# Kernel tuning notes

Measured on AMD Instinct MI355X. Metric: run time of the kernel, lower is better.

Reference implementation:

```python
import jax, jax.numpy as jnp
import numpy as np

GAMMA = 1.0          # softmin temperature (module default gamma=1.0)
BIG = 1e30           # finite stand-in for +inf (avoids NaN grads through masked cells)
# step_sizes = [[1,0],[0,1],[1,1]], global_step_weights = [1,1,1], normalization='N'

B, N, M, D = 64, 512, 512, 128


def setup_inputs() -> dict:
    key = jax.random.key(0)
    k1, k2 = jax.random.split(key)
    X = jax.random.normal(k1, (B, N, D), dtype=jnp.float32)
    Y = jax.random.normal(k2, (B, M, D), dtype=jnp.float32)
    return {"X": X, "Y": Y}


def _mse_cost(X, Y):
    # C[b,n,m] = mean_d (X[b,n,d] - Y[b,m,d])^2, expanded to avoid a BxNxMxD intermediate
    d = X.shape[-1]
    x2 = jnp.sum(X * X, axis=-1)                      # (B, N)
    y2 = jnp.sum(Y * Y, axis=-1)                      # (B, M)
    xy = jnp.einsum('bnd,bmd->bnm', X, Y)             # (B, N, M)
    return (x2[:, :, None] + y2[:, None, :] - 2.0 * xy) / d


def _soft_dtw(C):
    # Soft-DTW DP via anti-diagonal wavefront scan.
    # R[n,m] = softmin_gamma(R[n-1,m]+c, R[n,m-1]+c, R[n-1,m-1]+c), R[0,0]=C[0,0]
    # (all global step weights are 1.0). Returns R[N-1, M-1] per batch element.
    b, n, m = C.shape
    i_idx = jnp.arange(n)
    ds = jnp.arange(n + m - 1)
    cols = ds[:, None] - i_idx[None, :]               # (n+m-1, n): col index on each diagonal
    valid = (cols >= 0) & (cols < m)
    colsc = jnp.clip(cols, 0, m - 1)
    Cs = C[:, i_idx[None, :], colsc]                  # (b, n+m-1, n) skewed cost
    Cs = jnp.where(valid[None], Cs, 0.0)
    Cs = jnp.transpose(Cs, (1, 0, 2))                 # (n+m-1, b, n)

    pad = jnp.full((b, 1), BIG, C.dtype)

    def shift(r):  # access index i-1 along the diagonal
        return jnp.concatenate([pad, r[:, :-1]], axis=1)

    def step(carry, inp):
        prev, prev2 = carry                           # diagonals d-1, d-2: (b, n)
        c, val, d = inp
        # candidates: steps (1,0), (0,1), (1,1)
        a = jnp.stack([shift(prev) + c, prev + c, shift(prev2) + c], axis=0)  # (3, b, n)
        mn = jax.lax.stop_gradient(jnp.min(a, axis=0))
        r = mn - GAMMA * jnp.log(jnp.sum(jnp.exp((mn - a) / GAMMA), axis=0))
        # start boundary condition (0,0) with W_start=1
        r = jnp.where((d == 0) & (i_idx[None, :] == 0), c, r)
        r = jnp.where(val[None, :], r, BIG)
        return (r, prev), None

    init = (jnp.full((b, n), BIG, C.dtype), jnp.full((b, n), BIG, C.dtype))
    (last, _), _ = jax.lax.scan(step, init, (Cs, valid, ds))
    # end boundary (N-1, M-1) with additive W_end=0
    return last[:, n - 1]


def reference(X, Y):
    C = _mse_cost(X, Y)
    cost = _soft_dtw(C)                               # (B,)
    # normalization='N': mean over batch of cost / N
    return jnp.mean(cost / X.shape[1])
```

## Files before the change

kernel.cpp:

```cpp
#include <hip/hip_runtime.h>
#include <math.h>

#define BATCH 64
#define NN 512
#define MM 512
#define DD 128
#define BIGF 1e30f
#define KLOG2E 1.442695040888963f
#define LN2F   0.693147180559945f
#define BIGK   (BIGF * KLOG2E)

#define NA 768
#define NP 256

typedef __attribute__((ext_vector_type(2))) float f32x2;
typedef __attribute__((ext_vector_type(4))) float f32x4;
typedef __attribute__((ext_vector_type(8))) short s16x8;

__device__ __forceinline__ unsigned short f2bf(float f) {
    unsigned u = __float_as_uint(f);
    u += 0x7FFFu + ((u >> 16) & 1u);
    return (unsigned short)(u >> 16);
}

#define LSI(A, IP) ((A) * 32 + ((IP) ^ ((A) & 31)))

__global__ __launch_bounds__(256) void cost_diag_mfma(const float* __restrict__ X,
                                                      const float* __restrict__ Y,
                                                      f32x2* __restrict__ Cd) {
    __shared__ alignas(16) short smem[2 * 64 * 128];
    __shared__ float x2s[64];
    __shared__ float y2s[64];
    short* Xbf = smem;
    short* Ybf = smem + 64 * 128;
    f32x2* Ls  = (f32x2*)smem;

    int b  = blockIdx.z;
    int ti = blockIdx.y * 64;
    int tj = blockIdx.x * 64;
    int t  = threadIdx.x;
    int l  = t & 63;
    int w  = t >> 6;

    const float* Xb = X + ((size_t)b * NN + ti) * DD;
    const float* Yb = Y + ((size_t)b * MM + tj) * DD;

    int rw  = t >> 4;
    int k8l = t & 15;
    float xs_acc[4], ys_acc[4];
    #pragma unroll
    for (int it = 0; it < 4; ++it) {
        int r = rw + it * 16;
        const float* sx = Xb + (size_t)r * DD + k8l * 8;
        const float* sy = Yb + (size_t)r * DD + k8l * 8;
        float4 x0 = *(const float4*)sx;
        float4 x1 = *(const float4*)(sx + 4);
        float4 y0 = *(const float4*)sy;
        float4 y1 = *(const float4*)(sy + 4);
        xs_acc[it] = x0.x*x0.x + x0.y*x0.y + x0.z*x0.z + x0.w*x0.w
                   + x1.x*x1.x + x1.y*x1.y + x1.z*x1.z + x1.w*x1.w;
        ys_acc[it] = y0.x*y0.x + y0.y*y0.y + y0.z*y0.z + y0.w*y0.w
                   + y1.x*y1.x + y1.y*y1.y + y1.z*y1.z + y1.w*y1.w;
        s16x8 xv, yv;
        xv[0] = (short)f2bf(x0.x); xv[1] = (short)f2bf(x0.y);
        xv[2] = (short)f2bf(x0.z); xv[3] = (short)f2bf(x0.w);
        xv[4] = (short)f2bf(x1.x); xv[5] = (short)f2bf(x1.y);
        xv[6] = (short)f2bf(x1.z); xv[7] = (short)f2bf(x1.w);
        yv[0] = (short)f2bf(y0.x); yv[1] = (short)f2bf(y0.y);
        yv[2] = (short)f2bf(y0.z); yv[3] = (short)f2bf(y0.w);
        yv[4] = (short)f2bf(y1.x); yv[5] = (short)f2bf(y1.y);
        yv[6] = (short)f2bf(y1.z); yv[7] = (short)f2bf(y1.w);
        int sw = (r * 16 + (k8l ^ (r & 7))) * 8;
        *(s16x8*)&Xbf[sw] = xv;
        *(s16x8*)&Ybf[sw] = yv;
    }
    #pragma unroll
    for (int it = 0; it < 4; ++it) {
        float xs = xs_acc[it], ys = ys_acc[it];
        #pragma unroll
        for (int m = 8; m >= 1; m >>= 1) {
            xs += __shfl_xor(xs, m, 16);
            ys += __shfl_xor(ys, m, 16);
        }
        if (k8l == 0) { x2s[rw + it * 16] = xs; y2s[rw + it * 16] = ys; }
    }
    __syncthreads();

    f32x4 acc0 = {0.f,0.f,0.f,0.f}, acc1 = acc0, acc2 = acc0, acc3 = acc0;
    int ar = 16 * w + (l & 15);
    int kb = l >> 4;
    int c0 = l & 15;
    #pragma unroll
    for (int kk = 0; kk < 4; ++kk) {
        int k8 = kk * 4 + kb;
        s16x8 af = *(const s16x8*)&Xbf[(ar * 16 + (k8 ^ (ar & 7))) * 8];
        s16x8 b0 = *(const s16x8*)&Ybf[((c0     ) * 16 + (k8 ^ ((c0     ) & 7))) * 8];
        s16x8 b1 = *(const s16x8*)&Ybf[((c0 + 16) * 16 + (k8 ^ ((c0 + 16) & 7))) * 8];
        s16x8 b2 = *(const s16x8*)&Ybf[((c0 + 32) * 16 + (k8 ^ ((c0 + 32) & 7))) * 8];
        s16x8 b3 = *(const s16x8*)&Ybf[((c0 + 48) * 16 + (k8 ^ ((c0 + 48) & 7))) * 8];
        acc0 = __builtin_amdgcn_mfma_f32_16x16x32_bf16(af, b0, acc0, 0, 0, 0);
        acc1 = __builtin_amdgcn_mfma_f32_16x16x32_bf16(af, b1, acc1, 0, 0, 0);
        acc2 = __builtin_amdgcn_mfma_f32_16x16x32_bf16(af, b2, acc2, 0, 0, 0);
        acc3 = __builtin_amdgcn_mfma_f32_16x16x32_bf16(af, b3, acc3, 0, 0, 0);
    }

    const float inv = KLOG2E / (float)DD;
    int i0l = 16 * w + (l >> 4) * 4;
    float4 xx = *(const float4*)&x2s[i0l];
    float yy0 = y2s[c0];
    float yy1 = y2s[16 + c0];
    float yy2 = y2s[32 + c0];
    float yy3 = y2s[48 + c0];

    __syncthreads();

    int ipl0 = i0l >> 1;
    #define WRT(ACC, YY, C) do {                                               \
        int jl = 16 * (C) + c0;                                                \
        float v0 = (xx.x + (YY) - 2.0f * (ACC)[0]) * inv;                      \
        float v1 = (xx.y + (YY) - 2.0f * (ACC)[1]) * inv;                      \
        float v2 = (xx.z + (YY) - 2.0f * (ACC)[2]) * inv;                      \
        float v3 = (xx.w + (YY) - 2.0f * (ACC)[3]) * inv;                      \
        Ls[LSI(ipl0 + jl, ipl0)]         = f32x2{v0, v1};                      \
        Ls[LSI(ipl0 + 1 + jl, ipl0 + 1)] = f32x2{v2, v3};                      \
    } while (0)
    WRT(acc0, yy0, 0); WRT(acc1, yy1, 1); WRT(acc2, yy2, 2); WRT(acc3, yy3, 3);
    #undef WRT
    __syncthreads();

    f32x2* Cdb = Cd + (size_t)b * (NA * NP);
    int base_a = (ti >> 1) + tj;
    int ipbase = (ti >> 1);
    #pragma unroll
    for (int k = 0; k < 12; ++k) {
        int f  = t + k * 256;
        int al = f >> 5;
        int il = f & 31;
        int d  = al - il;
        if ((unsigned)d < 64u)
            Cdb[(size_t)(base_a + al) * NP + ipbase + il] = Ls[LSI(al, il)];
    }
}

#define RING 8
#define KCH 16
#define ESK 15
#define NITER 51

__global__ __launch_bounds__(256, 1) void sdtw_diag_kernel(const f32x2* __restrict__ Cd,
                                                           float* __restrict__ part) {
    int b = blockIdx.x;
    int p = threadIdx.x;
    int l = p & 63;
    int w = p >> 6;
    int wm1 = (w == 0) ? 0 : (w - 1);
    int wsk = ESK * w;
    int off = p + wsk;
    const char* CbL = (const char*)Cd + (size_t)b * (NA * NP * 8) + p * 8;

    __shared__ alignas(16) f32x2 buf[2][4][KCH];

    if (p < 128) ((f32x2*)buf)[p] = f32x2{BIGK, 1.0f};
    __syncthreads();

    float ps0 = BIGK, pq0 = 1.0f;
    float ps1 = BIGK, pq1 = 1.0f;
    float nbc_s = BIGK, nbc_q = 1.0f;
    float nbp_s = BIGK, nbp_q = 1.0f;
    f32x2 carry = {BIGK, 1.0f};

    f32x2 b0, b1, b2, b3, b4, b5, b6, b7, b8, b9, b10, b11, b12, b13, b14, b15;
    b0=b1=b2=b3=b4=b5=b6=b7=b8=b9=b10=b11=b12=b13=b14=b15 = f32x2{BIGK, 1.0f};

    f32x2 r0, r1, r2, r3, r4, r5, r6, r7;

#define LOADPD(REG, AV) do {                                                   \
    int a_ = (AV);                                                             \
    a_ = a_ < 0 ? 0 : (a_ > NA - 1 ? NA - 1 : a_);                             \
    const char* pa_ = CbL + (unsigned)a_ * (NP * 8u);                          \
    asm volatile("global_load_dwordx2 %0, %1, off"                             \
                 : "=&v"(REG) : "v"(pa_) : "memory");                          \
} while (0)

    LOADPD(r0, 0 - wsk); LOADPD(r1, 1 - wsk); LOADPD(r2, 2 - wsk);
    LOADPD(r3, 3 - wsk); LOADPD(r4, 4 - wsk); LOADPD(r5, 5 - wsk);
    LOADPD(r6, 6 - wsk); LOADPD(r7, 7 - wsk);

#define STEPD(REG, SIG, BS, UBX, UBY, DBX, DBY) do {                           \
    int s_ = sbase + (SIG);                                                    \
    int j_ = s_ - off;                                                         \
    f32x2 cc;                                                                  \
    asm volatile("s_waitcnt vmcnt(7)" : "=v"(cc) : "0"(REG));                  \
    float su, qu, sd2, qd;                                                     \
    if (l == 0) {                                                              \
        if (w == 0) { su = BIGK; qu = 1.0f;                                    \
                      sd2 = (s_ == 0) ? 0.0f : BIGK; qd = 1.0f; }              \
        else        { su = (UBX); qu = (UBY); sd2 = (DBX); qd = (DBY); }       \
    } else { su = nbc_s; qu = nbc_q; sd2 = nbp_s; qd = nbp_q; }                \
    if ((unsigned)j_ < 512u) {                                                 \
        float lAs = ps0, lAq = pq0;                                            \
        float m1;                                                              \
        asm("v_min3_f32 %0, %1, %2, %3" : "=v"(m1) : "v"(su), "v"(lAs), "v"(sd2)); \
        float eu, el, ed;                                                      \
        asm("v_exp_f32 %0, %1" : "=v"(eu) : "v"(m1 - su));                     \
        asm("v_exp_f32 %0, %1" : "=v"(el) : "v"(m1 - lAs));                    \
        asm("v_exp_f32 %0, %1" : "=v"(ed) : "v"(m1 - sd2));                    \
        float qA = __builtin_fmaf(qu, eu, __builtin_fmaf(lAq, el, qd * ed));   \
        float sA = cc.x + m1;                                                  \
        float m2;                                                              \
        asm("v_min3_f32 %0, %1, %2, %3" : "=v"(m2) : "v"(sA), "v"(ps1), "v"(lAs)); \
        float fu, fl, fd;                                                      \
        asm("v_exp_f32 %0, %1" : "=v"(fu) : "v"(m2 - sA));                     \
        asm("v_exp_f32 %0, %1" : "=v"(fl) : "v"(m2 - ps1));                    \
        asm("v_exp_f32 %0, %1" : "=v"(fd) : "v"(m2 - lAs));                    \
        float qB = __builtin_fmaf(qA, fu, __builtin_fmaf(pq1, fl, lAq * fd));  \
        float sB = cc.y + m2;                                                  \
        ps0 = sA; pq0 = qA; ps1 = sB; pq1 = qB;                                \
    }                                                                          \
    BS = f32x2{ps1, pq1};                                                      \
    float shs_, shq_;                                                          \
    asm("v_mov_b32_dpp %0, %2 wave_shr:1 row_mask:0xf bank_mask:0xf\n\t"       \
        "v_mov_b32_dpp %1, %3 wave_shr:1 row_mask:0xf bank_mask:0xf"           \
        : "=v"(shs_), "=v"(shq_) : "v"(ps1), "v"(pq1));                        \
    nbp_s = nbc_s; nbp_q = nbc_q;                                              \
    nbc_s = shs_;  nbc_q = shq_;                                               \
    LOADPD(REG, s_ + RING - wsk);                                              \
} while (0)

#define RENORMD(S, Q) do {                                                     \
    int e_ = (__float_as_int(Q) >> 23) - 127;                                  \
    Q = __int_as_float(__float_as_int(Q) - (e_ << 23));                        \
    S = S - (float)e_;                                                         \
} while (0)

    for (int I = 0; I < NITER; ++I) {
        asm volatile("s_waitcnt lgkmcnt(0)" ::: "memory");
        __builtin_amdgcn_s_barrier();
        asm volatile("" ::: "memory");
        const f32x4* rq = (const f32x4*)&buf[(I + 1) & 1][wm1][0];
        f32x4 c0 = rq[0], c1 = rq[1], c2 = rq[2], c3 = rq[3];
        f32x4 c4 = rq[4], c5 = rq[5], c6 = rq[6], c7 = rq[7];
        int sbase = I * KCH;
        STEPD(r0, 0,  b0,  c0[0], c0[1], carry.x, carry.y);
        STEPD(r1, 1,  b1,  c0[2], c0[3], c0[0], c0[1]);
        STEPD(r2, 2,  b2,  c1[0], c1[1], c0[2], c0[3]);
        STEPD(r3, 3,  b3,  c1[2], c1[3], c1[0], c1[1]);
        STEPD(r4, 4,  b4,  c2[0], c2[1], c1[2], c1[3]);
        STEPD(r5, 5,  b5,  c2[2], c2[3], c2[0], c2[1]);
        STEPD(r6, 6,  b6,  c3[0], c3[1], c2[2], c2[3]);
        STEPD(r7, 7,  b7,  c3[2], c3[3], c3[0], c3[1]);
        STEPD(r0, 8,  b8,  c4[0], c4[1], c3[2], c3[3]);
        STEPD(r1, 9,  b9,  c4[2], c4[3], c4[0], c4[1]);
        STEPD(r2, 10, b10, c5[0], c5[1], c4[2], c4[3]);
        STEPD(r3, 11, b11, c5[2], c5[3], c5[0], c5[1]);
        STEPD(r4, 12, b12, c6[0], c6[1], c5[2], c5[3]);
        STEPD(r5, 13, b13, c6[2], c6[3], c6[0], c6[1]);
        STEPD(r6, 14, b14, c7[0], c7[1], c6[2], c6[3]);
        STEPD(r7, 15, b15, c7[2], c7[3], c7[0], c7[1]);
        carry = f32x2{c7[2], c7[3]};
        if (l == 63) {
            f32x2* wbp = &buf[I & 1][w][0];
            wbp[0]  = b0;  wbp[1]  = b1;  wbp[2]  = b2;  wbp[3]  = b3;
            wbp[4]  = b4;  wbp[5]  = b5;  wbp[6]  = b6;  wbp[7]  = b7;
            wbp[8]  = b8;  wbp[9]  = b9;  wbp[10] = b10; wbp[11] = b11;
            wbp[12] = b12; wbp[13] = b13; wbp[14] = b14; wbp[15] = b15;
        }
        RENORMD(ps0, pq0);
        RENORMD(ps1, pq1);
    }

    if (p == 255) {
        float lg;
        asm("v_log_f32 %0, %1" : "=v"(lg) : "v"(pq1));
        part[b] = (ps1 - lg) * LN2F;
    }
#undef STEPD
#undef LOADPD
#undef RENORMD
}

__global__ __launch_bounds__(64) void reduce_kernel(const float* __restrict__ part,
                                                    float* __restrict__ out) {
    int l = threadIdx.x;
    float v = part[l];
    #pragma unroll
    for (int m = 32; m >= 1; m >>= 1) v += __shfl_xor(v, m, 64);
    if (l == 0) out[0] = v / (float)(BATCH * NN);
}

extern "C" void kernel_launch(void* const* d_in, const int* in_sizes, int n_in,
                              void* d_out, int out_size, void* d_ws, size_t ws_size,
                              hipStream_t stream) {
    const float* X = (const float*)d_in[0];
    const float* Y = (const float*)d_in[1];
    float* out = (float*)d_out;
    char* ws = (char*)d_ws;

    const size_t cdBytes = (size_t)BATCH * NA * NP * 8;

    f32x2* Cd   = (f32x2*)ws;
    float* part = (float*)(ws + cdBytes);

    dim3 g(MM / 64, NN / 64, BATCH);
    cost_diag_mfma<<<g, 256, 0, stream>>>(X, Y, Cd);

    sdtw_diag_kernel<<<BATCH, 256, 0, stream>>>(Cd, part);

    reduce_kernel<<<1, 64, 0, stream>>>(part, out);
}
```

Before: 161.4 us.

## Software-pipeline soft-DTW step: split min/exp chain from deferred q accumulation

Each diagonal step is split into a scalar-offset chain (min3 plus exps) and a separate q-value accumulation. The q-value accumulation for step s is deferred and interleaved with the exp chain of step s+1, and a flush handles the chunk's last step. The aim is to shorten the serial dependency latency per step by overlapping the FMA chain with the next step's transcendental work, and the DPP neighbour exchange of q is shifted by one step to match. It also drops the occupancy hint in the launch bounds. The change adds more live registers and fragile ordering of boundary values across waves and chunks.

```diff
diff --git a/kernel.cpp b/kernel.cpp
--- a/kernel.cpp
+++ b/kernel.cpp
@@ -147,8 +147,8 @@
 #define ESK 15
 #define NITER 51
 
-__global__ __launch_bounds__(256, 1) void sdtw_diag_kernel(const f32x2* __restrict__ Cd,
-                                                           float* __restrict__ part) {
+__global__ __launch_bounds__(256) void sdtw_diag_kernel(const f32x2* __restrict__ Cd,
+                                                        float* __restrict__ part) {
     int b = blockIdx.x;
     int p = threadIdx.x;
     int l = p & 63;
@@ -168,6 +168,8 @@
     float nbc_s = BIGK, nbc_q = 1.0f;
     float nbp_s = BIGK, nbp_q = 1.0f;
     f32x2 carry = {BIGK, 1.0f};
+    float qfl = 1.0f;
+    float eS = 0.f, lS = 0.f, dS = 0.f, fS = 0.f, gS = 0.f, hS = 0.f;
 
     f32x2 b0, b1, b2, b3, b4, b5, b6, b7, b8, b9, b10, b11, b12, b13, b14, b15;
     b0=b1=b2=b3=b4=b5=b6=b7=b8=b9=b10=b11=b12=b13=b14=b15 = f32x2{BIGK, 1.0f};
@@ -186,45 +188,83 @@
     LOADPD(r3, 3 - wsk); LOADPD(r4, 4 - wsk); LOADPD(r5, 5 - wsk);
     LOADPD(r6, 6 - wsk); LOADPD(r7, 7 - wsk);
 
-#define STEPD(REG, SIG, BS, UBX, UBY, DBX, DBY) do {                           \
+#define SCHAIN(CC, S_, SUX, SDX) do {                                          \
+    float su_, sd_;                                                            \
+    if (l == 0) {                                                              \
+        if (w == 0) { su_ = BIGK; sd_ = ((S_) == 0) ? 0.0f : BIGK; }           \
+        else        { su_ = (SUX); sd_ = (SDX); }                              \
+    } else { su_ = nbc_s; sd_ = nbp_s; }                                       \
+    if ((unsigned)j_ < 512u) {                                                 \
+        float lAs = ps0;                                                       \
+        float m1;                                                              \
+        asm("v_min3_f32 %0, %1, %2, %3" : "=v"(m1) : "v"(su_), "v"(lAs), "v"(sd_)); \
+        asm("v_exp_f32 %0, %1" : "=v"(eS) : "v"(m1 - su_));                    \
+        asm("v_exp_f32 %0, %1" : "=v"(lS) : "v"(m1 - lAs));                    \
+        asm("v_exp_f32 %0, %1" : "=v"(dS) : "v"(m1 - sd_));                    \
+        float sA = (CC).x + m1;                                                \
+        float m2;                                                              \
+        asm("v_min3_f32 %0, %1, %2, %3" : "=v"(m2) : "v"(sA), "v"(ps1), "v"(lAs)); \
+        asm("v_exp_f32 %0, %1" : "=v"(fS) : "v"(m2 - sA));                     \
+        asm("v_exp_f32 %0, %1" : "=v"(gS) : "v"(m2 - ps1));                    \
+        asm("v_exp_f32 %0, %1" : "=v"(hS) : "v"(m2 - lAs));                    \
+        ps0 = sA;                                                              \
+        ps1 = (CC).y + m2;                                                     \
+    }                                                                          \
+} while (0)
+
+#define QRESOLVE(JR, QUY, QDY) do {                                            \
+    float qu_, qd_;                                                            \
+    if (l == 0) {                                                              \
+        if (w == 0) { qu_ = 1.0f; qd_ = 1.0f; }                                \
+        else        { qu_ = (QUY); qd_ = (QDY); }                              \
+    } else { qu_ = nbc_q; qd_ = nbp_q; }                                       \
+    if ((unsigned)(JR) < 512u) {                                               \
+        float qAo = pq0;                                                       \
+        float qA = __builtin_fmaf(qu_, eS, __builtin_fmaf(pq0, lS, qd_ * dS)); \
+        float qB = __builtin_fmaf(qA, fS, __builtin_fmaf(pq1, gS, qAo * hS));  \
+        pq0 = qA; pq1 = qB;                                                    \
+    }                                                                          \
+} while (0)
+
+#define STEPN(REG, SIG, BSS, BSQ, SUX, SDX, QUY, QDY) do {                     \
     int s_ = sbase + (SIG);                                                    \
     int j_ = s_ - off;                                                         \
     f32x2 cc;                                                                  \
     asm volatile("s_waitcnt vmcnt(7)" : "=v"(cc) : "0"(REG));                  \
-    float su, qu, sd2, qd;                                                     \
-    if (l == 0) {                                                              \
-        if (w == 0) { su = BIGK; qu = 1.0f;                                    \
-                      sd2 = (s_ == 0) ? 0.0f : BIGK; qd = 1.0f; }              \
-        else        { su = (UBX); qu = (UBY); sd2 = (DBX); qd = (DBY); }       \
-    } else { su = nbc_s; qu = nbc_q; sd2 = nbp_s; qd = nbp_q; }                \
-    if ((unsigned)j_ < 512u) {                                                 \
-        float lAs = ps0, lAq = pq0;                                            \
-        float m1;                                                              \
-        asm("v_min3_f32 %0, %1, %2, %3" : "=v"(m1) : "v"(su), "v"(lAs), "v"(sd2)); \
-        float eu, el, ed;                                                      \
-        asm("v_exp_f32 %0, %1" : "=v"(eu) : "v"(m1 - su));                     \
-        asm("v_exp_f32 %0, %1" : "=v"(el) : "v"(m1 - lAs));                    \
-        asm("v_exp_f32 %0, %1" : "=v"(ed) : "v"(m1 - sd2));                    \
-        float qA = __builtin_fmaf(qu, eu, __builtin_fmaf(lAq, el, qd * ed));   \
-        float sA = cc.x + m1;                                                  \
-        float m2;                                                              \
-        asm("v_min3_f32 %0, %1, %2, %3" : "=v"(m2) : "v"(sA), "v"(ps1), "v"(lAs)); \
-        float fu, fl, fd;                                                      \
-        asm("v_exp_f32 %0, %1" : "=v"(fu) : "v"(m2 - sA));                     \
-        asm("v_exp_f32 %0, %1" : "=v"(fl) : "v"(m2 - ps1));                    \
-        asm("v_exp_f32 %0, %1" : "=v"(fd) : "v"(m2 - lAs));                    \
-        float qB = __builtin_fmaf(qA, fu, __builtin_fmaf(pq1, fl, lAq * fd));  \
-        float sB = cc.y + m2;                                                  \
-        ps0 = sA; pq0 = qA; ps1 = sB; pq1 = qB;                                \
-    }                                                                          \
-    BS = f32x2{ps1, pq1};                                                      \
+    QRESOLVE(j_ - 1, QUY, QDY);                                                \
+    BSQ.y = pq1;                                                               \
+    SCHAIN(cc, s_, SUX, SDX);                                                  \
+    BSS.x = ps1;                                                               \
     float shs_, shq_;                                                          \
     asm("v_mov_b32_dpp %0, %2 wave_shr:1 row_mask:0xf bank_mask:0xf\n\t"       \
         "v_mov_b32_dpp %1, %3 wave_shr:1 row_mask:0xf bank_mask:0xf"           \
         : "=v"(shs_), "=v"(shq_) : "v"(ps1), "v"(pq1));                        \
-    nbp_s = nbc_s; nbp_q = nbc_q;                                              \
-    nbc_s = shs_;  nbc_q = shq_;                                               \
+    nbp_s = nbc_s; nbc_s = shs_;                                               \
+    nbp_q = nbc_q; nbc_q = shq_;                                               \
     LOADPD(REG, s_ + RING - wsk);                                              \
+} while (0)
+
+#define STEP0(REG, BSS) do {                                                   \
+    int s_ = sbase;                                                            \
+    int j_ = s_ - off;                                                         \
+    f32x2 cc;                                                                  \
+    asm volatile("s_waitcnt vmcnt(7)" : "=v"(cc) : "0"(REG));                  \
+    SCHAIN(cc, s_, c0[0], carry.x);                                            \
+    BSS.x = ps1;                                                               \
+    float shs_;                                                                \
+    asm("v_mov_b32_dpp %0, %1 wave_shr:1 row_mask:0xf bank_mask:0xf"           \
+        : "=v"(shs_) : "v"(ps1));                                              \
+    nbp_s = nbc_s; nbc_s = shs_;                                               \
+    nbp_q = nbc_q; nbc_q = qfl;                                                \
+    LOADPD(REG, s_ + RING - wsk);                                              \
+} while (0)
+
+#define FLUSHQ() do {                                                          \
+    int jr_ = sbase + 15 - off;                                                \
+    QRESOLVE(jr_, c7[3], c7[1]);                                               \
+    b15.y = pq1;                                                               \
+    asm("v_mov_b32_dpp %0, %1 wave_shr:1 row_mask:0xf bank_mask:0xf"           \
+        : "=v"(qfl) : "v"(pq1));                                               \
 } while (0)
 
 #define RENORMD(S, Q) do {                                                     \
@@ -241,22 +281,23 @@
         f32x4 c0 = rq[0], c1 = rq[1], c2 = rq[2], c3 = rq[3];
         f32x4 c4 = rq[4], c5 = rq[5], c6 = rq[6], c7 = rq[7];
         int sbase = I * KCH;
-        STEPD(r0, 0,  b0,  c0[0], c0[1], carry.x, carry.y);
-        STEPD(r1, 1,  b1,  c0[2], c0[3], c0[0], c0[1]);
-        STEPD(r2, 2,  b2,  c1[0], c1[1], c0[2], c0[3]);
-        STEPD(r3, 3,  b3,  c1[2], c1[3], c1[0], c1[1]);
-        STEPD(r4, 4,  b4,  c2[0], c2[1], c1[2], c1[3]);
-        STEPD(r5, 5,  b5,  c2[2], c2[3], c2[0], c2[1]);
-        STEPD(r6, 6,  b6,  c3[0], c3[1], c2[2], c2[3]);
-        STEPD(r7, 7,  b7,  c3[2], c3[3], c3[0], c3[1]);
-        STEPD(r0, 8,  b8,  c4[0], c4[1], c3[2], c3[3]);
-        STEPD(r1, 9,  b9,  c4[2], c4[3], c4[0], c4[1]);
-        STEPD(r2, 10, b10, c5[0], c5[1], c4[2], c4[3]);
-        STEPD(r3, 11, b11, c5[2], c5[3], c5[0], c5[1]);
-        STEPD(r4, 12, b12, c6[0], c6[1], c5[2], c5[3]);
-        STEPD(r5, 13, b13, c6[2], c6[3], c6[0], c6[1]);
-        STEPD(r6, 14, b14, c7[0], c7[1], c6[2], c6[3]);
-        STEPD(r7, 15, b15, c7[2], c7[3], c7[0], c7[1]);
+        STEP0(r0, b0);
+        STEPN(r1, 1,  b1,  b0,  c0[2], c0[0], c0[1], carry.y);
+        STEPN(r2, 2,  b2,  b1,  c1[0], c0[2], c0[3], c0[1]);
+        STEPN(r3, 3,  b3,  b2,  c1[2], c1[0], c1[1], c0[3]);
+        STEPN(r4, 4,  b4,  b3,  c2[0], c1[2], c1[3], c1[1]);
+        STEPN(r5, 5,  b5,  b4,  c2[2], c2[0], c2[1], c1[3]);
+        STEPN(r6, 6,  b6,  b5,  c3[0], c2[2], c2[3], c2[1]);
+        STEPN(r7, 7,  b7,  b6,  c3[2], c3[0], c3[1], c2[3]);
+        STEPN(r0, 8,  b8,  b7,  c4[0], c3[2], c3[3], c3[1]);
+        STEPN(r1, 9,  b9,  b8,  c4[2], c4[0], c4[1], c3[3]);
+        STEPN(r2, 10, b10, b9,  c5[0], c4[2], c4[3], c4[1]);
+        STEPN(r3, 11, b11, b10, c5[2], c5[0], c5[1], c4[3]);
+        STEPN(r4, 12, b12, b11, c6[0], c5[2], c5[3], c5[1]);
+        STEPN(r5, 13, b13, b12, c6[2], c6[0], c6[1], c5[3]);
+        STEPN(r6, 14, b14, b13, c7[0], c6[2], c6[3], c6[1]);
+        STEPN(r7, 15, b15, b14, c7[2], c7[0], c7[1], c6[3]);
+        FLUSHQ();
         carry = f32x2{c7[2], c7[3]};
         if (l == 63) {
             f32x2* wbp = &buf[I & 1][w][0];
@@ -274,7 +315,11 @@
         asm("v_log_f32 %0, %1" : "=v"(lg) : "v"(pq1));
         part[b] = (ps1 - lg) * LN2F;
     }
-#undef STEPD
+#undef STEPN
+#undef STEP0
+#undef FLUSHQ
+#undef QRESOLVE
+#undef SCHAIN
 #undef LOADPD
 #undef RENORMD
 }
```

Measured after the change: 145.5 us, median of 2. -9.9%, faster.
